# Kernel tuning notes

Hardware: AMD Instinct MI355X
Metric: run time of the kernel (lower is better)

Reference implementation:

```python
import jax, jax.numpy as jnp
import numpy as np

SIZE = 256
K_SIGN = 100000.0
EPS = 1e-05

# mesh: torch.meshgrid default indexing='ij', stacked, flattened, / size -> (size^2, 2)
_MESH = jnp.stack(jnp.meshgrid(jnp.arange(SIZE, dtype=jnp.float32),
                               jnp.arange(SIZE, dtype=jnp.float32),
                               indexing='ij'), axis=-1).reshape(-1, 2) / SIZE


def setup_inputs() -> dict:
    key = jax.random.key(0)
    # contour values must lie in [0, 1]
    contour = jax.random.uniform(key, (2, 2, 64, 2), dtype=jnp.float32)
    return {"contour": contour}


def reference(contour) -> jnp.ndarray:
    b, n, k, _ = contour.shape
    c = contour.reshape(b * n, 1, k, 2)          # (bn, 1, K, 2)
    mesh = _MESH[None, :, None, :]               # (1, S^2, 1, 2)
    diff = c - mesh                              # (bn, S^2, K, 2)

    norm_diff = jnp.linalg.norm(diff, axis=-1)   # (bn, S^2, K)
    min_diff = jnp.min(norm_diff, axis=2).reshape(b * n, SIZE, SIZE)

    roll_diff = jnp.roll(diff, -1, axis=2)       # next vertex along K
    # torch: sign = (diff * roll(roll_diff,1,dims=3)); sign[...,1]-sign[...,0]
    #       = diff_y*roll_x - diff_x*roll_y
    cross = diff[..., 1] * roll_diff[..., 0] - diff[..., 0] * roll_diff[..., 1]
    sign = jnp.tanh(K_SIGN * cross)

    nd = jnp.clip(norm_diff, EPS)
    nr = jnp.clip(jnp.linalg.norm(roll_diff, axis=-1), EPS)
    scalar_product = jnp.sum(diff * roll_diff, axis=-1)
    cos_ang = jnp.clip(scalar_product / (nd * nr), -1.0 + EPS, 1.0 - EPS)
    angles = jnp.arccos(cos_ang)

    winding = jnp.abs(jnp.sum(sign * angles, axis=2)) / (2.0 * jnp.pi)  # (bn, S^2)
    resize = winding.reshape(b * n, SIZE, SIZE)

    prod = resize * min_diff
    dmap = prod / jnp.max(prod)                  # global max normalization
    return dmap.reshape(b, n, SIZE, SIZE)
```

## Files before the change

### kernel.cpp

```cpp
#include <hip/hip_runtime.h>
#include <math.h>

#define SZ 256
#define KPTS 64
#define GROUPS 4
#define SEGS_PER (KPTS / GROUPS)
#define NBLK (4 * SZ * 2)
#define K_SIGN 100000.0f
#define EPS_C 1e-5f
#define INV_2PI 0.15915494309189535f
#define PI_F 3.14159265358979323846f
#define K2_LOG2E 288539.00817779269f

__device__ __forceinline__ float fast_rcp(float x)  { return __builtin_amdgcn_rcpf(x); }
__device__ __forceinline__ float fast_sqrt(float x) { return __builtin_amdgcn_sqrtf(x); }
__device__ __forceinline__ float fast_rsq(float x)  { return __builtin_amdgcn_rsqf(x); }
__device__ __forceinline__ float fast_exp2(float x) { return __builtin_amdgcn_exp2f(x); }

__device__ __forceinline__ float fast_tanh_k(float cross) {
    float t = fast_exp2(K2_LOG2E * cross);
    return fmaf(-2.0f, fast_rcp(t + 1.0f), 1.0f);
}

__device__ __forceinline__ float fast_acos(float x) {
    float ax = fabsf(x);
    float s  = fast_sqrt(1.0f - ax);
    float p  = s * fmaf(ax, fmaf(ax, fmaf(ax, -0.0187292994f, 0.0742610037f),
                                  -0.2121143937f), 1.5707288f);
    return (x >= 0.0f) ? p : (PI_F - p);
}


__global__ __launch_bounds__(256) void contour_prod_kernel(
    const float* __restrict__ contour,
    float* __restrict__ out,
    float* __restrict__ ws)
{
    __shared__ float2 cpt[KPTS + 1];
    __shared__ float wred[4];

    const int blk = blockIdx.x;
    const int jq  = blk & 1;
    const int i   = (blk >> 1) & 255;
    const int bn  = blk >> 9;

    const int t = threadIdx.x;
    if (t < KPTS) {
        float2 p = ((const float2*)contour)[bn * KPTS + t];
        cpt[t] = p;
        if (t == 0) cpt[KPTS] = p;
    }
    __syncthreads();

    const int g    = t & 3;
    const int slot = t >> 2;
    const int j0   = (jq << 7) + (slot << 1);

    const float mx  = (float)i  * (1.0f / (float)SZ);
    const float my0 = (float)j0 * (1.0f / (float)SZ);
    const float my1 = my0 + (1.0f / (float)SZ);

    const int base = g * SEGS_PER;

    float2 cp = cpt[base];
    float dxc  = cp.x - mx;
    float dyc0 = cp.y - my0;
    float dyc1 = cp.y - my1;
    const float dx2c = dxc * dxc;
    float n2c0 = fmaf(dyc0, dyc0, dx2c);
    float n2c1 = fmaf(dyc1, dyc1, dx2c);
    float mn0  = n2c0, mn1 = n2c1;
    float acc0 = 0.0f, acc1 = 0.0f;

    #pragma unroll
    for (int kk = 0; kk < SEGS_PER; ++kk) {
        const float2 cn = cpt[base + kk + 1];
        const float dxn  = cn.x - mx;
        const float dyn0 = cn.y - my0;
        const float dyn1 = cn.y - my1;
        const float dx2  = dxn * dxn;
        const float n2n0 = fmaf(dyn0, dyn0, dx2);
        const float n2n1 = fmaf(dyn1, dyn1, dx2);
        mn0 = fminf(mn0, n2n0);
        mn1 = fminf(mn1, n2n1);

        const float dd = dxc * dxn;
        const float cross0 = fmaf(dyc0, dxn, -dxc * dyn0);
        const float cross1 = fmaf(dyc1, dxn, -dxc * dyn1);
        const float dot0   = fmaf(dyc0, dyn0, dd);
        const float dot1   = fmaf(dyc1, dyn1, dd);

        float ca0 = dot0 * fast_rsq(n2c0 * n2n0);
        float ca1 = dot1 * fast_rsq(n2c1 * n2n1);
        ca0 = fminf(fmaxf(ca0, -1.0f + EPS_C), 1.0f - EPS_C);
        ca1 = fminf(fmaxf(ca1, -1.0f + EPS_C), 1.0f - EPS_C);
        const float ang0 = fast_acos(ca0);
        const float ang1 = fast_acos(ca1);

        const float s0 = fast_tanh_k(cross0);
        const float s1 = fast_tanh_k(cross1);

        acc0 = fmaf(s0, ang0, acc0);
        acc1 = fmaf(s1, ang1, acc1);

        dxc = dxn;
        dyc0 = dyn0; dyc1 = dyn1;
        n2c0 = n2n0; n2c1 = n2n1;
    }

    acc0 += __shfl_xor(acc0, 1, 64);
    acc0 += __shfl_xor(acc0, 2, 64);
    acc1 += __shfl_xor(acc1, 1, 64);
    acc1 += __shfl_xor(acc1, 2, 64);
    mn0 = fminf(mn0, __shfl_xor(mn0, 1, 64));
    mn0 = fminf(mn0, __shfl_xor(mn0, 2, 64));
    mn1 = fminf(mn1, __shfl_xor(mn1, 1, 64));
    mn1 = fminf(mn1, __shfl_xor(mn1, 2, 64));

    const float prod0 = fabsf(acc0) * INV_2PI * fast_sqrt(mn0);
    const float prod1 = fabsf(acc1) * INV_2PI * fast_sqrt(mn1);
    if (g == 0) {
        float2 pv = make_float2(prod0, prod1);
        ((float2*)out)[(((bn << 8) + i) << 7) + (jq << 6) + slot] = pv;
    }

    float wmax = fmaxf(prod0, prod1);
    #pragma unroll
    for (int off = 32; off > 0; off >>= 1)
        wmax = fmaxf(wmax, __shfl_down(wmax, off, 64));
    if ((t & 63) == 0) wred[t >> 6] = wmax;
    __syncthreads();
    if (t == 0)
        ws[blk] = fmaxf(fmaxf(wred[0], wred[1]), fmaxf(wred[2], wred[3]));
}

__global__ __launch_bounds__(256) void contour_norm_kernel(
    float4* __restrict__ out,
    const float* __restrict__ ws)
{
    __shared__ float wred[4];
    __shared__ float smax;

    const int t = threadIdx.x;
    const float4* w4 = (const float4*)ws;

    float m = 0.0f;
    {
        float4 a = w4[t];
        float4 b = w4[t + 256];
        m = fmaxf(fmaxf(fmaxf(a.x, a.y), fmaxf(a.z, a.w)),
                  fmaxf(fmaxf(b.x, b.y), fmaxf(b.z, b.w)));
    }
    #pragma unroll
    for (int off = 32; off > 0; off >>= 1)
        m = fmaxf(m, __shfl_down(m, off, 64));
    if ((t & 63) == 0) wred[t >> 6] = m;
    __syncthreads();
    if (t == 0)
        smax = fmaxf(fmaxf(wred[0], wred[1]), fmaxf(wred[2], wred[3]));
    __syncthreads();

    const float inv = 1.0f / smax;
    const int idx = blockIdx.x * 256 + t;
    float4 v = out[idx];
    v.x *= inv; v.y *= inv; v.z *= inv; v.w *= inv;
    out[idx] = v;
}

extern "C" void kernel_launch(void* const* d_in, const int* in_sizes, int n_in,
                              void* d_out, int out_size, void* d_ws, size_t ws_size,
                              hipStream_t stream)
{
    const float* contour = (const float*)d_in[0];
    float* out = (float*)d_out;
    float* ws  = (float*)d_ws;

    contour_prod_kernel<<<NBLK, SZ, 0, stream>>>(contour, out, ws);
    contour_norm_kernel<<<out_size / 4 / 256, 256, 0, stream>>>((float4*)out, ws);
}
```

Before: 21.94 us.

## Replace acos with atan2 of cross/dot, use DPP reductions, per-wave max

Computes each angle as atan2(|cross|, dot) with a polynomial instead of an rsq-normalised cosine followed by acos, so squared norms are no longer carried between iterations. Two reciprocals are merged into one shared reciprocal for the pair of pixels, in both the angle and the tanh sign path. Lane reductions now use DPP moves, and the block-level max via shared memory and barrier is dropped in favour of writing one max per wave, so the norm kernel reads four times as many partials. Clamping the angle bounds instead of cos changes the numerics slightly, and the DPP row-shift/broadcast reduction relies on exact lane semantics.

New measurement: 25.98 us. 18.4% more time.

```diff
diff --git a/kernel.cpp b/kernel.cpp
--- a/kernel.cpp
+++ b/kernel.cpp
@@ -7,37 +7,52 @@
 #define SEGS_PER (KPTS / GROUPS)
 #define NBLK (4 * SZ * 2)
 #define K_SIGN 100000.0f
-#define EPS_C 1e-5f
 #define INV_2PI 0.15915494309189535f
 #define PI_F 3.14159265358979323846f
+#define HALFPI_F 1.57079632679489662f
 #define K2_LOG2E 288539.00817779269f
+#define ANG_LO 4.4721373e-3f
+#define ANG_HI 3.1371205e-0f
+#define AT1 0.99997726f
+#define AT3 -0.33262347f
+#define AT5 0.19354346f
+#define AT7 -0.11643287f
+#define AT9 0.05265332f
 
 __device__ __forceinline__ float fast_rcp(float x)  { return __builtin_amdgcn_rcpf(x); }
 __device__ __forceinline__ float fast_sqrt(float x) { return __builtin_amdgcn_sqrtf(x); }
-__device__ __forceinline__ float fast_rsq(float x)  { return __builtin_amdgcn_rsqf(x); }
 __device__ __forceinline__ float fast_exp2(float x) { return __builtin_amdgcn_exp2f(x); }
 
-__device__ __forceinline__ float fast_tanh_k(float cross) {
-    float t = fast_exp2(K2_LOG2E * cross);
-    return fmaf(-2.0f, fast_rcp(t + 1.0f), 1.0f);
+template <int CTRL>
+__device__ __forceinline__ float dpp_mov(float v) {
+    return __int_as_float(__builtin_amdgcn_update_dpp(
+        __float_as_int(v), __float_as_int(v), CTRL, 0xF, 0xF, false));
 }
+#define DPP_XOR1   0xB1
+#define DPP_XOR2   0x4E
+#define DPP_SHR4   0x114
+#define DPP_SHR8   0x118
+#define DPP_BC15   0x142
+#define DPP_BC31   0x143
 
-__device__ __forceinline__ float fast_acos(float x) {
-    float ax = fabsf(x);
-    float s  = fast_sqrt(1.0f - ax);
-    float p  = s * fmaf(ax, fmaf(ax, fmaf(ax, -0.0187292994f, 0.0742610037f),
-                                  -0.2121143937f), 1.5707288f);
-    return (x >= 0.0f) ? p : (PI_F - p);
+__device__ __forceinline__ float fast_atan2pos(float y, float x, float mo_r) {
+    const float n = fminf(fabsf(x), y);
+    const float t = n * mo_r;
+    const float s = t * t;
+    float p = fmaf(s, fmaf(s, fmaf(s, fmaf(s, AT9, AT7), AT5), AT3), AT1);
+    p *= t;
+    float r = (y > fabsf(x)) ? (HALFPI_F - p) : p;
+    r = (x < 0.0f) ? (PI_F - r) : r;
+    return r;
 }
 
 
-__global__ __launch_bounds__(256) void contour_prod_kernel(
+__global__ __launch_bounds__(256, 8) void contour_prod_kernel(
     const float* __restrict__ contour,
     float* __restrict__ out,
     float* __restrict__ ws)
 {
     __shared__ float2 cpt[KPTS + 1];
-    __shared__ float wred[4];
 
     const int blk = blockIdx.x;
     const int jq  = blk & 1;
@@ -67,9 +82,8 @@
     float dyc0 = cp.y - my0;
     float dyc1 = cp.y - my1;
     const float dx2c = dxc * dxc;
-    float n2c0 = fmaf(dyc0, dyc0, dx2c);
-    float n2c1 = fmaf(dyc1, dyc1, dx2c);
-    float mn0  = n2c0, mn1 = n2c1;
+    float mn0  = fmaf(dyc0, dyc0, dx2c);
+    float mn1  = fmaf(dyc1, dyc1, dx2c);
     float acc0 = 0.0f, acc1 = 0.0f;
 
     #pragma unroll
@@ -79,59 +93,62 @@
         const float dyn0 = cn.y - my0;
         const float dyn1 = cn.y - my1;
         const float dx2  = dxn * dxn;
-        const float n2n0 = fmaf(dyn0, dyn0, dx2);
-        const float n2n1 = fmaf(dyn1, dyn1, dx2);
-        mn0 = fminf(mn0, n2n0);
-        mn1 = fminf(mn1, n2n1);
+        mn0 = fminf(mn0, fmaf(dyn0, dyn0, dx2));
+        mn1 = fminf(mn1, fmaf(dyn1, dyn1, dx2));
 
         const float dd = dxc * dxn;
         const float cross0 = fmaf(dyc0, dxn, -dxc * dyn0);
         const float cross1 = fmaf(dyc1, dxn, -dxc * dyn1);
         const float dot0   = fmaf(dyc0, dyn0, dd);
         const float dot1   = fmaf(dyc1, dyn1, dd);
+        const float y0 = fabsf(cross0);
+        const float y1 = fabsf(cross1);
 
-        float ca0 = dot0 * fast_rsq(n2c0 * n2n0);
-        float ca1 = dot1 * fast_rsq(n2c1 * n2n1);
-        ca0 = fminf(fmaxf(ca0, -1.0f + EPS_C), 1.0f - EPS_C);
-        ca1 = fminf(fmaxf(ca1, -1.0f + EPS_C), 1.0f - EPS_C);
-        const float ang0 = fast_acos(ca0);
-        const float ang1 = fast_acos(ca1);
+        const float m0 = fmaxf(fabsf(dot0), y0);
+        const float m1 = fmaxf(fabsf(dot1), y1);
+        const float rr = fast_rcp(m0 * m1);
+        float ang0 = fast_atan2pos(y0, dot0, m1 * rr);
+        float ang1 = fast_atan2pos(y1, dot1, m0 * rr);
+        ang0 = fminf(fmaxf(ang0, ANG_LO), ANG_HI);
+        ang1 = fminf(fmaxf(ang1, ANG_LO), ANG_HI);
 
-        const float s0 = fast_tanh_k(cross0);
-        const float s1 = fast_tanh_k(cross1);
+        const float e0 = fast_exp2(fminf(K2_LOG2E * cross0, 100.0f));
+        const float e1 = fast_exp2(fminf(K2_LOG2E * cross1, 100.0f));
+        const float f0 = e0 + 1.0f;
+        const float f1 = e1 + 1.0f;
+        const float r2 = fast_rcp(f0 * f1);
+        const float s0 = fmaf(-2.0f, f1 * r2, 1.0f);
+        const float s1 = fmaf(-2.0f, f0 * r2, 1.0f);
 
         acc0 = fmaf(s0, ang0, acc0);
         acc1 = fmaf(s1, ang1, acc1);
 
-        dxc = dxn;
-        dyc0 = dyn0; dyc1 = dyn1;
-        n2c0 = n2n0; n2c1 = n2n1;
+        dxc = dxn; dyc0 = dyn0; dyc1 = dyn1;
     }
 
-    acc0 += __shfl_xor(acc0, 1, 64);
-    acc0 += __shfl_xor(acc0, 2, 64);
-    acc1 += __shfl_xor(acc1, 1, 64);
-    acc1 += __shfl_xor(acc1, 2, 64);
-    mn0 = fminf(mn0, __shfl_xor(mn0, 1, 64));
-    mn0 = fminf(mn0, __shfl_xor(mn0, 2, 64));
-    mn1 = fminf(mn1, __shfl_xor(mn1, 1, 64));
-    mn1 = fminf(mn1, __shfl_xor(mn1, 2, 64));
+    acc0 += dpp_mov<DPP_XOR1>(acc0);
+    acc0 += dpp_mov<DPP_XOR2>(acc0);
+    acc1 += dpp_mov<DPP_XOR1>(acc1);
+    acc1 += dpp_mov<DPP_XOR2>(acc1);
+    mn0 = fminf(mn0, dpp_mov<DPP_XOR1>(mn0));
+    mn0 = fminf(mn0, dpp_mov<DPP_XOR2>(mn0));
+    mn1 = fminf(mn1, dpp_mov<DPP_XOR1>(mn1));
+    mn1 = fminf(mn1, dpp_mov<DPP_XOR2>(mn1));
 
     const float prod0 = fabsf(acc0) * INV_2PI * fast_sqrt(mn0);
     const float prod1 = fabsf(acc1) * INV_2PI * fast_sqrt(mn1);
     if (g == 0) {
-        float2 pv = make_float2(prod0, prod1);
-        ((float2*)out)[(((bn << 8) + i) << 7) + (jq << 6) + slot] = pv;
+        ((float2*)out)[(((bn << 8) + i) << 7) + (jq << 6) + slot] =
+            make_float2(prod0, prod1);
     }
 
-    float wmax = fmaxf(prod0, prod1);
-    #pragma unroll
-    for (int off = 32; off > 0; off >>= 1)
-        wmax = fmaxf(wmax, __shfl_down(wmax, off, 64));
-    if ((t & 63) == 0) wred[t >> 6] = wmax;
-    __syncthreads();
-    if (t == 0)
-        ws[blk] = fmaxf(fmaxf(wred[0], wred[1]), fmaxf(wred[2], wred[3]));
+    float wm = fmaxf(prod0, prod1);
+    wm = fmaxf(wm, dpp_mov<DPP_SHR4>(wm));
+    wm = fmaxf(wm, dpp_mov<DPP_SHR8>(wm));
+    wm = fmaxf(wm, dpp_mov<DPP_BC15>(wm));
+    wm = fmaxf(wm, dpp_mov<DPP_BC31>(wm));
+    if ((t & 63) == 63)
+        ws[(blk << 2) + (t >> 6)] = wm;
 }
 
 __global__ __launch_bounds__(256) void contour_norm_kernel(
@@ -145,11 +162,10 @@
     const float4* w4 = (const float4*)ws;
 
     float m = 0.0f;
-    {
-        float4 a = w4[t];
-        float4 b = w4[t + 256];
-        m = fmaxf(fmaxf(fmaxf(a.x, a.y), fmaxf(a.z, a.w)),
-                  fmaxf(fmaxf(b.x, b.y), fmaxf(b.z, b.w)));
+    #pragma unroll
+    for (int r = 0; r < 8; ++r) {
+        float4 v = w4[t + (r << 8)];
+        m = fmaxf(m, fmaxf(fmaxf(v.x, v.y), fmaxf(v.z, v.w)));
     }
     #pragma unroll
     for (int off = 32; off > 0; off >>= 1)
```
